# Performance work log

Hardware: AMD Instinct MI355X
Metric: run time of the kernel (lower is better)

## Reference

```python
import jax, jax.numpy as jnp
import numpy as np

G = 64      # num graphs
N = 1024    # nodes per graph (equal-sized graphs)
D_IN, D_H, D_OUT = 128, 256, 10


def setup_inputs() -> dict:
    key = jax.random.key(0)
    k1, k2, k3, k4, k5 = jax.random.split(key, 5)
    x = jax.random.normal(k1, (G * N, D_IN), dtype=jnp.float32)
    batch = jnp.repeat(jnp.arange(G, dtype=jnp.int64), N)  # sorted graph ids
    lim1 = 1.0 / np.sqrt(D_IN)
    lim2 = 1.0 / np.sqrt(D_H)
    W1 = jax.random.uniform(k2, (D_IN, D_H), minval=-lim1, maxval=lim1, dtype=jnp.float32)
    b1 = jax.random.uniform(k3, (D_H,), minval=-lim1, maxval=lim1, dtype=jnp.float32)
    W2 = jax.random.uniform(k4, (D_H, D_OUT), minval=-lim2, maxval=lim2, dtype=jnp.float32)
    b2 = jax.random.uniform(k5, (D_OUT,), minval=-lim2, maxval=lim2, dtype=jnp.float32)
    return {"x": x, "batch": batch, "W1": W1, "b1": b1, "W2": W2, "b2": b2}


def reference(x, batch, W1, b1, W2, b2):
    # Equal-sized graphs: reshape node dim into [G, N, d] (batch is sorted).
    xg = x.reshape(G, N, D_IN)
    # Cosine-similarity adjacency per graph, zero diagonal (from RAW features).
    xn = xg * jax.lax.rsqrt(jnp.sum(xg * xg, axis=-1, keepdims=True) + 1e-24)
    adj = jnp.einsum('gnd,gmd->gnm', xn, xn)            # [G, N, N]
    adj = adj * (1.0 - jnp.eye(N, dtype=adj.dtype))
    # fc1 + relu on node features, then adjacency propagation.
    h = jax.nn.relu(xg @ W1 + b1)                       # [G, N, D_H]
    h = jnp.einsum('gnm,gmd->gnd', adj, h)              # [G, N, D_H]
    # fc2, global mean pool over nodes, log-softmax over classes.
    out = h @ W2 + b2                                   # [G, N, D_OUT]
    pooled = jnp.mean(out, axis=1)                      # [G, D_OUT]
    return jax.nn.log_softmax(pooled, axis=-1)
```

## Files before the change

### kernel.cpp

```cpp
#include <hip/hip_runtime.h>
#include <hip/hip_bf16.h>
#include <string.h>

#define G_ 64
#define N_ 1024
#define DIN 128
#define DH 256
#define DOUT 10

typedef float floatx4 __attribute__((ext_vector_type(4)));
typedef short shortx8 __attribute__((ext_vector_type(8)));

__device__ __forceinline__ ushort f2bf(float f) {
  unsigned u = __builtin_bit_cast(unsigned, f);
  unsigned r = (u + 0x7FFFu + ((u >> 16) & 1u)) >> 16;
  return (ushort)r;
}
__device__ __forceinline__ float bflo(unsigned q) {
  return __builtin_bit_cast(float, q << 16);
}
__device__ __forceinline__ float bfhi(unsigned q) {
  return __builtin_bit_cast(float, q & 0xFFFF0000u);
}

__global__ __launch_bounds__(256) void k0_w1t(
    const float* __restrict__ W1, ushort* __restrict__ w1t) {
  const int idx = blockIdx.x * 256 + threadIdx.x;
  const int k = idx >> 8, d = idx & 255;
  w1t[d * DIN + k] = f2bf(W1[k * DH + d]);
}

__global__ __launch_bounds__(256) void k1_norm_u(
    const float* __restrict__ x, float* __restrict__ norminv,
    float* __restrict__ u, ushort* __restrict__ xb) {
  const int g = blockIdx.x >> 4;
  const int wave = threadIdx.x >> 6;
  const int lane = threadIdx.x & 63;
  __shared__ float red[4][DIN];
  float a0 = 0.f, a1 = 0.f;
  const int mbase = blockIdx.x * 64 + wave * 16;
  for (int i = 0; i < 16; ++i) {
    const int m = mbase + i;
    const float2 v = ((const float2*)(x + (size_t)m * DIN))[lane];
    float ss = v.x * v.x + v.y * v.y;
    #pragma unroll
    for (int off = 32; off; off >>= 1) ss += __shfl_xor(ss, off, 64);
    const float ninv = rsqrtf(ss + 1e-24f);
    if (lane == 0) norminv[m] = ninv;
    ((unsigned*)xb)[(size_t)m * (DIN / 2) + lane] =
        (unsigned)f2bf(v.x) | ((unsigned)f2bf(v.y) << 16);
    a0 = fmaf(v.x, ninv, a0);
    a1 = fmaf(v.y, ninv, a1);
  }
  red[wave][2 * lane] = a0;
  red[wave][2 * lane + 1] = a1;
  __syncthreads();
  if (threadIdx.x < DIN) {
    const float t = red[0][threadIdx.x] + red[1][threadIdx.x] +
                    red[2][threadIdx.x] + red[3][threadIdx.x];
    atomicAdd(&u[g * DIN + threadIdx.x], t);
  }
}

__global__ __launch_bounds__(256) void k2_mfma(
    const ushort* __restrict__ xb, const ushort* __restrict__ w1t,
    const float* __restrict__ b1, const float* __restrict__ norminv,
    const float* __restrict__ u, float* __restrict__ hw) {
  const int g = blockIdx.x >> 3;
  const int mb = (blockIdx.x & 7) << 7;
  const int lane = threadIdx.x & 63;
  const int wave = threadIdx.x >> 6;
  const int quad = lane >> 4;
  const int l16 = lane & 15;
  __shared__ float u_lds[DIN];
  __shared__ float s_lds[128];

  if (threadIdx.x < DIN) u_lds[threadIdx.x] = u[g * DIN + threadIdx.x];
  __syncthreads();

  {
    const int nd = threadIdx.x >> 1;
    const int half = threadIdx.x & 1;
    const size_t m = (size_t)(g << 10) + mb + nd;
    const uint4* xr = (const uint4*)(xb + m * DIN + half * 64);
    float p = 0.f;
    #pragma unroll
    for (int j = 0; j < 8; ++j) {
      const uint4 q = xr[j];
      const float* ub = &u_lds[half * 64 + j * 8];
      p = fmaf(bflo(q.x), ub[0], p); p = fmaf(bfhi(q.x), ub[1], p);
      p = fmaf(bflo(q.y), ub[2], p); p = fmaf(bfhi(q.y), ub[3], p);
      p = fmaf(bflo(q.z), ub[4], p); p = fmaf(bfhi(q.z), ub[5], p);
      p = fmaf(bflo(q.w), ub[6], p); p = fmaf(bfhi(q.w), ub[7], p);
    }
    p += __shfl_xor(p, 1, 64);
    if (!half) s_lds[nd] = p * norminv[m] - 1.0f;
  }
  __syncthreads();

  shortx8 bfr[4][4];
  #pragma unroll
  for (int dt = 0; dt < 4; ++dt) {
    const int d = (wave << 6) + (dt << 4) + l16;
    #pragma unroll
    for (int kt = 0; kt < 4; ++kt)
      bfr[dt][kt] = *(const shortx8*)(w1t + (size_t)d * DIN + (kt << 5) + (quad << 3));
  }
  float b1v[4];
  #pragma unroll
  for (int dt = 0; dt < 4; ++dt) b1v[dt] = b1[(wave << 6) + (dt << 4) + l16];

  float wsum[4] = {0.f, 0.f, 0.f, 0.f};
  for (int mt = 0; mt < 8; ++mt) {
    const ushort* ar = xb + ((size_t)(g << 10) + mb + (mt << 4) + l16) * DIN;
    shortx8 af[4];
    #pragma unroll
    for (int kt = 0; kt < 4; ++kt)
      af[kt] = *(const shortx8*)(ar + (kt << 5) + (quad << 3));

    floatx4 acc[4] = {{0.f, 0.f, 0.f, 0.f}, {0.f, 0.f, 0.f, 0.f},
                      {0.f, 0.f, 0.f, 0.f}, {0.f, 0.f, 0.f, 0.f}};
    #pragma unroll
    for (int kt = 0; kt < 4; ++kt)
      #pragma unroll
      for (int dt = 0; dt < 4; ++dt)
        acc[dt] = __builtin_amdgcn_mfma_f32_16x16x32_bf16(af[kt], bfr[dt][kt],
                                                          acc[dt], 0, 0, 0);
    #pragma unroll
    for (int dt = 0; dt < 4; ++dt) {
      float bs = 0.f;
      #pragma unroll
      for (int r = 0; r < 4; ++r) {
        const float h = fmaxf(acc[dt][r] + b1v[dt], 0.f);
        bs = fmaf(s_lds[(mt << 4) + (quad << 2) + r], h, bs);
      }
      wsum[dt] += bs;
    }
  }
  #pragma unroll
  for (int dt = 0; dt < 4; ++dt) {
    float w = wsum[dt];
    w += __shfl_xor(w, 16, 64);
    w += __shfl_xor(w, 32, 64);
    if (quad == 0)
      atomicAdd(&hw[g * DH + (wave << 6) + (dt << 4) + l16], w);
  }
}

__global__ __launch_bounds__(64) void k3_head(
    const float* __restrict__ hw, const float* __restrict__ W2,
    const float* __restrict__ b2, float* __restrict__ out) {
  const int g = blockIdx.x;
  const int t = threadIdx.x;
  __shared__ float partial[40];
  __shared__ float p[DOUT];
  if (t < 40) {
    const int c = t % 10, q = t / 10;
    const float* hg = hw + g * DH + q * 64;
    float a = 0.f;
    #pragma unroll
    for (int k = 0; k < 64; ++k) a = fmaf(hg[k], W2[(q * 64 + k) * DOUT + c], a);
    partial[t] = a;
  }
  __syncthreads();
  if (t < DOUT) {
    p[t] = (partial[t] + partial[t + 10] + partial[t + 20] + partial[t + 30]) *
               (1.0f / N_) + b2[t];
  }
  __syncthreads();
  if (t < DOUT) {
    float mx = p[0];
    #pragma unroll
    for (int c = 1; c < DOUT; ++c) mx = fmaxf(mx, p[c]);
    float se = 0.f;
    #pragma unroll
    for (int c = 0; c < DOUT; ++c) se += expf(p[c] - mx);
    out[g * DOUT + t] = p[t] - (mx + logf(se));
  }
}

extern "C" void kernel_launch(void* const* d_in, const int* in_sizes, int n_in,
                              void* d_out, int out_size, void* d_ws, size_t ws_size,
                              hipStream_t stream) {
  const float* x  = (const float*)d_in[0];
  const float* W1 = (const float*)d_in[2];
  const float* b1 = (const float*)d_in[3];
  const float* W2 = (const float*)d_in[4];
  const float* b2 = (const float*)d_in[5];
  float* out = (float*)d_out;

  float* hw = (float*)d_ws;
  float* u  = hw + G_ * DH;
  float* norminv = u + G_ * DIN;
  ushort* xb  = (ushort*)(norminv + G_ * N_);
  ushort* w1t = xb + (size_t)G_ * N_ * DIN;

  hipMemsetAsync(d_ws, 0, (size_t)(G_ * DH + G_ * DIN) * sizeof(float), stream);
  k0_w1t<<<DIN, 256, 0, stream>>>(W1, w1t);
  k1_norm_u<<<G_ * 16, 256, 0, stream>>>(x, norminv, u, xb);
  k2_mfma<<<G_ * 8, 256, 0, stream>>>(xb, w1t, b1, norminv, u, hw);
  k3_head<<<G_, 64, 0, stream>>>(hw, W2, b2, out);
}
```

Measured before the change: 111.7 us.

## Fuse weight transpose into norm kernel, replace atomics with partial buffers, drop memset

The W1 transpose/convert is merged into the normalization kernel as extra blocks, which removes one launch. The global atomics for u and hw become per-block partial buffers that the next kernel sums, so the memset is no longer needed. The norm kernel now loads float4 per lane, and the MFMA kernel uses twice as many blocks with half the rows each for better occupancy. In exchange, the partial-sum reads add a little extra traffic.

```diff
diff --git a/kernel.cpp b/kernel.cpp
--- a/kernel.cpp
+++ b/kernel.cpp
@@ -1,6 +1,5 @@
 #include <hip/hip_runtime.h>
 #include <hip/hip_bf16.h>
-#include <string.h>
 
 #define G_ 64
 #define N_ 1024
@@ -23,95 +22,114 @@
   return __builtin_bit_cast(float, q & 0xFFFF0000u);
 }
 
-__global__ __launch_bounds__(256) void k0_w1t(
-    const float* __restrict__ W1, ushort* __restrict__ w1t) {
-  const int idx = blockIdx.x * 256 + threadIdx.x;
-  const int k = idx >> 8, d = idx & 255;
-  w1t[d * DIN + k] = f2bf(W1[k * DH + d]);
-}
-
-__global__ __launch_bounds__(256) void k1_norm_u(
-    const float* __restrict__ x, float* __restrict__ norminv,
-    float* __restrict__ u, ushort* __restrict__ xb) {
-  const int g = blockIdx.x >> 4;
-  const int wave = threadIdx.x >> 6;
-  const int lane = threadIdx.x & 63;
-  __shared__ float red[4][DIN];
-  float a0 = 0.f, a1 = 0.f;
+__global__ __launch_bounds__(256) void k1_fused(
+    const float* __restrict__ x, const float* __restrict__ W1,
+    float* __restrict__ norminv, float* __restrict__ u_part,
+    ushort* __restrict__ xb, ushort* __restrict__ w1t) {
+  if (blockIdx.x >= 1024) {
+    const int wb = blockIdx.x - 1024;
+    #pragma unroll
+    for (int i = 0; i < 2; ++i) {
+      const int idx = wb * 512 + i * 256 + threadIdx.x;
+      const int k = idx >> 8, d = idx & 255;
+      w1t[d * DIN + k] = f2bf(W1[k * DH + d]);
+    }
+    return;
+  }
+  const int tid = threadIdx.x;
+  const int wave = tid >> 6;
+  const int lane = tid & 63;
+  const int half = lane >> 5;
+  const int l32 = lane & 31;
+  __shared__ float red[8][DIN];
+  float a0 = 0.f, a1 = 0.f, a2 = 0.f, a3 = 0.f;
   const int mbase = blockIdx.x * 64 + wave * 16;
-  for (int i = 0; i < 16; ++i) {
-    const int m = mbase + i;
-    const float2 v = ((const float2*)(x + (size_t)m * DIN))[lane];
-    float ss = v.x * v.x + v.y * v.y;
-    #pragma unroll
-    for (int off = 32; off; off >>= 1) ss += __shfl_xor(ss, off, 64);
+  #pragma unroll
+  for (int i = 0; i < 8; ++i) {
+    const int m = mbase + i * 2 + half;
+    const float4 v = ((const float4*)(x + (size_t)m * DIN))[l32];
+    float ss = v.x * v.x + v.y * v.y + v.z * v.z + v.w * v.w;
+    #pragma unroll
+    for (int off = 16; off; off >>= 1) ss += __shfl_xor(ss, off, 64);
     const float ninv = rsqrtf(ss + 1e-24f);
-    if (lane == 0) norminv[m] = ninv;
-    ((unsigned*)xb)[(size_t)m * (DIN / 2) + lane] =
-        (unsigned)f2bf(v.x) | ((unsigned)f2bf(v.y) << 16);
+    if (l32 == 0) norminv[m] = ninv;
+    uint2 pk;
+    pk.x = (unsigned)f2bf(v.x) | ((unsigned)f2bf(v.y) << 16);
+    pk.y = (unsigned)f2bf(v.z) | ((unsigned)f2bf(v.w) << 16);
+    ((uint2*)(xb + (size_t)m * DIN))[l32] = pk;
     a0 = fmaf(v.x, ninv, a0);
     a1 = fmaf(v.y, ninv, a1);
-  }
-  red[wave][2 * lane] = a0;
-  red[wave][2 * lane + 1] = a1;
-  __syncthreads();
-  if (threadIdx.x < DIN) {
-    const float t = red[0][threadIdx.x] + red[1][threadIdx.x] +
-                    red[2][threadIdx.x] + red[3][threadIdx.x];
-    atomicAdd(&u[g * DIN + threadIdx.x], t);
+    a2 = fmaf(v.z, ninv, a2);
+    a3 = fmaf(v.w, ninv, a3);
+  }
+  *(float4*)&red[tid >> 5][l32 * 4] = make_float4(a0, a1, a2, a3);
+  __syncthreads();
+  if (tid < DIN) {
+    float t = 0.f;
+    #pragma unroll
+    for (int r = 0; r < 8; ++r) t += red[r][tid];
+    u_part[blockIdx.x * DIN + tid] = t;
   }
 }
 
 __global__ __launch_bounds__(256) void k2_mfma(
     const ushort* __restrict__ xb, const ushort* __restrict__ w1t,
     const float* __restrict__ b1, const float* __restrict__ norminv,
-    const float* __restrict__ u, float* __restrict__ hw) {
-  const int g = blockIdx.x >> 3;
-  const int mb = (blockIdx.x & 7) << 7;
-  const int lane = threadIdx.x & 63;
-  const int wave = threadIdx.x >> 6;
+    const float* __restrict__ u_part, float* __restrict__ hw_part) {
+  const int g = blockIdx.x >> 4;
+  const int mb = (blockIdx.x & 15) << 6;
+  const int tid = threadIdx.x;
+  const int lane = tid & 63;
+  const int wave = tid >> 6;
   const int quad = lane >> 4;
   const int l16 = lane & 15;
   __shared__ float u_lds[DIN];
-  __shared__ float s_lds[128];
-
-  if (threadIdx.x < DIN) u_lds[threadIdx.x] = u[g * DIN + threadIdx.x];
+  __shared__ float s_lds[64];
+
+  if (tid < DIN) {
+    float t = 0.f;
+    const float* up = u_part + (size_t)(g << 4) * DIN + tid;
+    #pragma unroll
+    for (int r = 0; r < 16; ++r) t += up[r * DIN];
+    u_lds[tid] = t;
+  }
   __syncthreads();
 
   {
-    const int nd = threadIdx.x >> 1;
-    const int half = threadIdx.x & 1;
+    const int nd = tid >> 2;
+    const int qq = tid & 3;
     const size_t m = (size_t)(g << 10) + mb + nd;
-    const uint4* xr = (const uint4*)(xb + m * DIN + half * 64);
+    const uint4* xr = (const uint4*)(xb + m * DIN + qq * 32);
     float p = 0.f;
     #pragma unroll
-    for (int j = 0; j < 8; ++j) {
+    for (int j = 0; j < 4; ++j) {
       const uint4 q = xr[j];
-      const float* ub = &u_lds[half * 64 + j * 8];
+      const float* ub = &u_lds[qq * 32 + j * 8];
       p = fmaf(bflo(q.x), ub[0], p); p = fmaf(bfhi(q.x), ub[1], p);
       p = fmaf(bflo(q.y), ub[2], p); p = fmaf(bfhi(q.y), ub[3], p);
       p = fmaf(bflo(q.z), ub[4], p); p = fmaf(bfhi(q.z), ub[5], p);
       p = fmaf(bflo(q.w), ub[6], p); p = fmaf(bfhi(q.w), ub[7], p);
     }
     p += __shfl_xor(p, 1, 64);
-    if (!half) s_lds[nd] = p * norminv[m] - 1.0f;
+    p += __shfl_xor(p, 2, 64);
+    if (qq == 0) s_lds[nd] = p * norminv[m] - 1.0f;
   }
   __syncthreads();
 
   shortx8 bfr[4][4];
+  float b1v[4];
   #pragma unroll
   for (int dt = 0; dt < 4; ++dt) {
     const int d = (wave << 6) + (dt << 4) + l16;
+    b1v[dt] = b1[d];
     #pragma unroll
     for (int kt = 0; kt < 4; ++kt)
       bfr[dt][kt] = *(const shortx8*)(w1t + (size_t)d * DIN + (kt << 5) + (quad << 3));
   }
-  float b1v[4];
-  #pragma unroll
-  for (int dt = 0; dt < 4; ++dt) b1v[dt] = b1[(wave << 6) + (dt << 4) + l16];
 
   float wsum[4] = {0.f, 0.f, 0.f, 0.f};
-  for (int mt = 0; mt < 8; ++mt) {
+  #pragma unroll
+  for (int mt = 0; mt < 4; ++mt) {
     const ushort* ar = xb + ((size_t)(g << 10) + mb + (mt << 4) + l16) * DIN;
     shortx8 af[4];
     #pragma unroll
@@ -143,20 +161,31 @@
     w += __shfl_xor(w, 16, 64);
     w += __shfl_xor(w, 32, 64);
     if (quad == 0)
-      atomicAdd(&hw[g * DH + (wave << 6) + (dt << 4) + l16], w);
+      hw_part[(size_t)blockIdx.x * DH + (wave << 6) + (dt << 4) + l16] = w;
   }
 }
 
 __global__ __launch_bounds__(64) void k3_head(
-    const float* __restrict__ hw, const float* __restrict__ W2,
+    const float* __restrict__ hw_part, const float* __restrict__ W2,
     const float* __restrict__ b2, float* __restrict__ out) {
   const int g = blockIdx.x;
   const int t = threadIdx.x;
+  __shared__ float hsum[DH];
   __shared__ float partial[40];
   __shared__ float p[DOUT];
+  {
+    float4 hs = make_float4(0.f, 0.f, 0.f, 0.f);
+    #pragma unroll
+    for (int r = 0; r < 16; ++r) {
+      const float4 v = ((const float4*)(hw_part + (size_t)((g << 4) + r) * DH))[t];
+      hs.x += v.x; hs.y += v.y; hs.z += v.z; hs.w += v.w;
+    }
+    ((float4*)hsum)[t] = hs;
+  }
+  __syncthreads();
   if (t < 40) {
     const int c = t % 10, q = t / 10;
-    const float* hg = hw + g * DH + q * 64;
+    const float* hg = hsum + q * 64;
     float a = 0.f;
     #pragma unroll
     for (int k = 0; k < 64; ++k) a = fmaf(hg[k], W2[(q * 64 + k) * DOUT + c], a);
@@ -189,15 +218,13 @@
   const float* b2 = (const float*)d_in[5];
   float* out = (float*)d_out;
 
-  float* hw = (float*)d_ws;
-  float* u  = hw + G_ * DH;
-  float* norminv = u + G_ * DIN;
-  ushort* xb  = (ushort*)(norminv + G_ * N_);
+  float* u_part  = (float*)d_ws;
+  float* hw_part = u_part + 1024 * DIN;
+  float* norminv = hw_part + 1024 * DH;
+  ushort* xb  = (ushort*)(norminv + (size_t)G_ * N_);
   ushort* w1t = xb + (size_t)G_ * N_ * DIN;
 
-  hipMemsetAsync(d_ws, 0, (size_t)(G_ * DH + G_ * DIN) * sizeof(float), stream);
-  k0_w1t<<<DIN, 256, 0, stream>>>(W1, w1t);
-  k1_norm_u<<<G_ * 16, 256, 0, stream>>>(x, norminv, u, xb);
-  k2_mfma<<<G_ * 8, 256, 0, stream>>>(xb, w1t, b1, norminv, u, hw);
-  k3_head<<<G_, 64, 0, stream>>>(hw, W2, b2, out);
-}
+  k1_fused<<<1024 + 64, 256, 0, stream>>>(x, W1, norminv, u_part, xb, w1t);
+  k2_mfma<<<G_ * 16, 256, 0, stream>>>(xb, w1t, b1, norminv, u_part, hw_part);
+  k3_head<<<G_, 64, 0, stream>>>(hw_part, W2, b2, out);
+}
```

After: 112.6 us. About the same (+0.8%).
